# Performance work log

Hardware: AMD Instinct MI355X
Metric: run time of the kernel (lower is better)

## Reference

```python
import jax, jax.numpy as jnp
from jax import lax
import numpy as np

SEQ_LEN, INPUT_DIM, NUM_HIDDEN, NUM_CLASSES, BATCH = 512, 64, 128, 10, 1024


def setup_inputs() -> dict:
    key = jax.random.key(0)
    ks = jax.random.split(key, 12)
    bound = float(np.sqrt(1.0 / NUM_HIDDEN))

    def u(k, shape):
        return jax.random.uniform(k, shape, jnp.float32, -bound, bound)

    return {
        "x": jax.random.normal(ks[0], (BATCH, SEQ_LEN, INPUT_DIM), jnp.float32),
        "W_gx": u(ks[1], (INPUT_DIM, NUM_HIDDEN)),
        "W_gh": u(ks[2], (NUM_HIDDEN, NUM_HIDDEN)),
        "W_ix": u(ks[3], (INPUT_DIM, NUM_HIDDEN)),
        "W_ih": u(ks[4], (NUM_HIDDEN, NUM_HIDDEN)),
        "W_fx": u(ks[5], (INPUT_DIM, NUM_HIDDEN)),
        "W_fh": u(ks[6], (NUM_HIDDEN, NUM_HIDDEN)),
        "W_ox": u(ks[7], (INPUT_DIM, NUM_HIDDEN)),
        "W_oh": u(ks[8], (NUM_HIDDEN, NUM_HIDDEN)),
        "W_ph": u(ks[9], (NUM_HIDDEN, NUM_CLASSES)),
        "b_g": jnp.zeros((NUM_HIDDEN,), jnp.float32),
        "b_i": jnp.zeros((NUM_HIDDEN,), jnp.float32),
        "b_f": jnp.ones((NUM_HIDDEN,), jnp.float32),  # forget-gate bias init to 1 as in original
        "b_o": jnp.zeros((NUM_HIDDEN,), jnp.float32),
        "b_p": jnp.zeros((NUM_CLASSES,), jnp.float32),
    }


def reference(x, W_gx, W_gh, W_ix, W_ih, W_fx, W_fh, W_ox, W_oh, W_ph,
              b_g, b_i, b_f, b_o, b_p):
    B, T, D = x.shape
    H = W_gh.shape[0]

    def step(carry, x_t):  # x_t: [B, D]
        h, c = carry
        g = jnp.tanh(x_t @ W_gx + h @ W_gh + b_g)
        i = jax.nn.sigmoid(x_t @ W_ix + h @ W_ih + b_i)
        f = jax.nn.sigmoid(x_t @ W_fx + h @ W_fh + b_f)
        o = jax.nn.sigmoid(x_t @ W_ox + h @ W_oh + b_o)
        c = g * i + c * f
        h = jnp.tanh(c) * o
        return (h, c), None

    h0 = jnp.zeros((B, H), x.dtype)
    c0 = jnp.zeros((B, H), x.dtype)
    (h, c), _ = lax.scan(step, (h0, c0), jnp.swapaxes(x, 0, 1))  # scan over time
    return h @ W_ph + b_p  # [B, num_classes]
```

## Files before the change

kernel.cpp:

```cpp
#include <hip/hip_runtime.h>

#define BATCH 1024
#define TSEQ  512
#define DIN   64
#define H     128
#define NCLS  10
#define BM    16
#define NTHREADS 512

typedef _Float16 h16;
typedef __attribute__((ext_vector_type(2))) _Float16 half2v;
typedef __attribute__((ext_vector_type(4))) _Float16 half4v;
typedef __attribute__((ext_vector_type(8))) _Float16 half8v;
typedef __attribute__((ext_vector_type(2))) float f32x2;
typedef __attribute__((ext_vector_type(4))) float f32x4;

__device__ __forceinline__ int stg_addr(int m, int k) {
    const int kg = k >> 3;
    return (((kg << 4) + (m ^ (kg & 7))) << 3) + (k & 7);
}

#define SCALE_G (-2.8853900817779268f)
#define SCALE_S (-1.4426950408889634f)

#define MFMA16(A, B, C) __builtin_amdgcn_mfma_f32_16x16x32_f16((A), (B), (C), 0, 0, 0)
#define EXP2(v) __builtin_amdgcn_exp2f(v)
#define RCP(v)  __builtin_amdgcn_rcpf(v)

#define CMATH(ACC, PAIR, CST, YCV)                                              \
  {                                                                             \
    f32x2 eg = { EXP2(ACC[0][2*(PAIR)]), EXP2(ACC[0][2*(PAIR)+1]) };            \
    f32x2 ei = { EXP2(ACC[1][2*(PAIR)]), EXP2(ACC[1][2*(PAIR)+1]) };            \
    f32x2 ef = { EXP2(ACC[2][2*(PAIR)]), EXP2(ACC[2][2*(PAIR)+1]) };            \
    f32x2 ag = one2 + eg, ai = one2 + ei, af = one2 + ef;                       \
    f32x2 dp  = ag * ai;                                                        \
    f32x2 t1  = (one2 - eg) * af;                                               \
    f32x2 num = CST * dp + t1;                                                  \
    f32x2 den = dp * af;                                                        \
    f32x2 rd  = { RCP(den[0]), RCP(den[1]) };                                   \
    f32x2 c   = num * rd;                                                       \
    CST = c;                                                                    \
    f32x2 yc = c * sg2;                                                         \
    YCV[0] = fminf(yc[0], 126.f);                                               \
    YCV[1] = fminf(yc[1], 126.f);                                               \
  }

#define HMATH(ACC, PAIR, YCV)                                                   \
  {                                                                             \
    f32x2 ec = { EXP2(YCV[0]), EXP2(YCV[1]) };                                  \
    f32x2 eo = { EXP2(ACC[3][2*(PAIR)]), EXP2(ACC[3][2*(PAIR)+1]) };            \
    f32x2 dh = (one2 + ec) * (one2 + eo);                                       \
    f32x2 nh = one2 - ec;                                                       \
    f32x2 rh = { RCP(dh[0]), RCP(dh[1]) };                                      \
    f32x2 hv = nh * rh;                                                         \
    hw[hwr[2*(PAIR)]]     = (h16)hv[0];                                         \
    hw[hwr[2*(PAIR) + 1]] = (h16)hv[1];                                         \
  }

__global__ __launch_bounds__(NTHREADS, 2)
void lstm_persist(const float* __restrict__ x,
                  const float* __restrict__ Wgx, const float* __restrict__ Wgh,
                  const float* __restrict__ Wix, const float* __restrict__ Wih,
                  const float* __restrict__ Wfx, const float* __restrict__ Wfh,
                  const float* __restrict__ Wox, const float* __restrict__ Woh,
                  const float* __restrict__ Wph,
                  const float* __restrict__ bg, const float* __restrict__ bi,
                  const float* __restrict__ bfg, const float* __restrict__ bo,
                  const float* __restrict__ bp,
                  float* __restrict__ out)
{
    __shared__ __align__(16) h16 hbuf[2][H * BM];
    __shared__ __align__(16) h16 xbuf[2][DIN * BM];

    const int tid  = threadIdx.x;
    const int wave = tid >> 6;
    const int lane = tid & 63;
    const int grp  = lane >> 4;
    const int ln   = lane & 15;
    const int b0   = blockIdx.x * BM;
    const int n    = (wave << 4) + ln;

    half8v bx[4][2];
    half8v bh[4][4];
    f32x4  bias_c[4];
    {
        const float* WX[4] = {Wgx, Wix, Wfx, Wox};
        const float* WH[4] = {Wgh, Wih, Wfh, Woh};
        const float* BB[4] = {bg, bi, bfg, bo};
        const float  SC[4] = {SCALE_G, SCALE_S, SCALE_S, SCALE_S};
        #pragma unroll
        for (int G = 0; G < 4; ++G) {
            #pragma unroll
            for (int s = 0; s < 2; ++s) {
                half8v v;
                #pragma unroll
                for (int j = 0; j < 8; ++j)
                    v[j] = (h16)(WX[G][(32*s + 8*grp + j) * H + n] * SC[G]);
                bx[G][s] = v;
            }
            #pragma unroll
            for (int s = 0; s < 4; ++s) {
                half8v v;
                #pragma unroll
                for (int j = 0; j < 8; ++j)
                    v[j] = (h16)(WH[G][(32*s + 8*grp + j) * H + n] * SC[G]);
                bh[G][s] = v;
            }
            const float bb = BB[G][n] * SC[G];
            bias_c[G] = (f32x4){bb, bb, bb, bb};
        }
    }

    const int ha0 = stg_addr(ln,      8 * grp);
    const int ha1 = stg_addr(ln, 32 + 8 * grp);
    const int ha2 = stg_addr(ln, 64 + 8 * grp);
    const int ha3 = stg_addr(ln, 96 + 8 * grp);
    const int xa0 = ha0;
    const int xa1 = ha1;
    int hwr[4];
    #pragma unroll
    for (int r = 0; r < 4; ++r) hwr[r] = stg_addr((grp << 2) + r, n);

    const int xm  = tid >> 5;
    const int xk0 = (tid & 31) << 1;
    const int xwr = stg_addr(xm, xk0);
    const float* xrow = x + (size_t)(b0 + xm) * TSEQ * DIN + xk0;

    const f32x2 one2 = {1.f, 1.f};
    const f32x2 sg2  = {SCALE_G, SCALE_G};

    *(half4v*)&hbuf[0][tid << 2] = (half4v)0;
    {
        f32x2 x0 = *(const f32x2*)xrow;
        *(half2v*)&xbuf[0][xwr] =
            __builtin_bit_cast(half2v, __builtin_amdgcn_cvt_pkrtz(x0[0], x0[1]));
    }
    __syncthreads();

    f32x4 accA[4], accB[4];
    {
        half8v xf0 = *(const half8v*)&xbuf[0][xa0];
        half8v xf1 = *(const half8v*)&xbuf[0][xa1];
        #pragma unroll
        for (int G = 0; G < 4; ++G) {
            accA[G] = MFMA16(xf0, bx[G][0], bias_c[G]);
            accA[G] = MFMA16(xf1, bx[G][1], accA[G]);
        }
    }
    __syncthreads();

    f32x2 xhold, xnew;
    {
        f32x2 x1 = *(const f32x2*)(xrow + DIN);
        *(half2v*)&xbuf[0][xwr] =
            __builtin_bit_cast(half2v, __builtin_amdgcn_cvt_pkrtz(x1[0], x1[1]));
        xhold = *(const f32x2*)(xrow + 2 * DIN);
        xnew  = *(const f32x2*)(xrow + 3 * DIN);
    }
    __syncthreads();

    f32x2 cst01 = {0.f, 0.f};
    f32x2 cst23 = {0.f, 0.f};

#define STEP(p_, tcur, ACCC, ACCN)                                              \
  {                                                                             \
                    \
    half8v xf0 = *(const half8v*)&xbuf[p_][xa0];                 \
    half8v xf1 = *(const half8v*)&xbuf[p_][xa1];                                \
    *(half2v*)&xbuf[p_ ^ 1][xwr] =                                              \
        __builtin_bit_cast(half2v, __builtin_amdgcn_cvt_pkrtz(xhold[0], xhold[1])); \
    xhold = xnew;                                                               \
    const int tpre = ((tcur) + 4 < TSEQ) ? (tcur) + 4 : TSEQ - 1;               \
    xnew = *(const f32x2*)(xrow + (size_t)tpre * DIN);                          \
    _Pragma("unroll")                                                           \
    for (int G = 0; G < 4; ++G) {                                               \
        ACCN[G] = MFMA16(xf0, bx[G][0], bias_c[G]);                             \
        ACCN[G] = MFMA16(xf1, bx[G][1], ACCN[G]);                               \
    }                                                                           \
    __syncthreads();                                                            \
                                                       \
    half8v ah0 = *(const half8v*)&hbuf[p_][ha0];                                \
    half8v ah1 = *(const half8v*)&hbuf[p_][ha1];                                \
    half8v ah2 = *(const half8v*)&hbuf[p_][ha2];                                \
    half8v ah3 = *(const half8v*)&hbuf[p_][ha3];                                \
                      \
    ACCC[0] = MFMA16(ah0, bh[0][0], ACCC[0]);                                   \
    ACCC[1] = MFMA16(ah0, bh[1][0], ACCC[1]);                                   \
    ACCC[2] = MFMA16(ah0, bh[2][0], ACCC[2]);                                   \
    ACCC[0] = MFMA16(ah1, bh[0][1], ACCC[0]);                                   \
    ACCC[1] = MFMA16(ah1, bh[1][1], ACCC[1]);                                   \
    ACCC[2] = MFMA16(ah1, bh[2][1], ACCC[2]);                                   \
    ACCC[0] = MFMA16(ah2, bh[0][2], ACCC[0]);                                   \
    ACCC[1] = MFMA16(ah2, bh[1][2], ACCC[1]);                                   \
    ACCC[2] = MFMA16(ah2, bh[2][2], ACCC[2]);                                   \
    ACCC[0] = MFMA16(ah3, bh[0][3], ACCC[0]);                                   \
    ACCC[1] = MFMA16(ah3, bh[1][3], ACCC[1]);                                   \
    ACCC[2] = MFMA16(ah3, bh[2][3], ACCC[2]);                                   \
                             \
    ACCC[3] = MFMA16(ah0, bh[3][0], ACCC[3]);                                   \
    ACCC[3] = MFMA16(ah1, bh[3][1], ACCC[3]);                                   \
    ACCC[3] = MFMA16(ah2, bh[3][2], ACCC[3]);                                   \
    ACCC[3] = MFMA16(ah3, bh[3][3], ACCC[3]);                                   \
    f32x2 yc0, yc1;                                                             \
    CMATH(ACCC, 0, cst01, yc0)                                                  \
    CMATH(ACCC, 1, cst23, yc1)                                                  \
    h16* hw = hbuf[p_ ^ 1];                                                     \
    HMATH(ACCC, 0, yc0)                                                         \
    HMATH(ACCC, 1, yc1)                                                         \
  }

    for (int t = 0; t < TSEQ; t += 2) {
        STEP(0, t,     accA, accB)
        STEP(1, t + 1, accB, accA)
    }
#undef STEP

    __syncthreads();
    if (tid < BM * NCLS) {
        const int m = tid / NCLS;
        const int cls = tid - m * NCLS;
        float s = bp[cls];
        #pragma unroll 8
        for (int k = 0; k < H; ++k) {
            float hvv = (float)hbuf[0][stg_addr(m, k)];
            s += hvv * Wph[k * NCLS + cls];
        }
        out[(size_t)(b0 + m) * NCLS + cls] = s;
    }
}

extern "C" void kernel_launch(void* const* d_in, const int* in_sizes, int n_in,
                              void* d_out, int out_size, void* d_ws, size_t ws_size,
                              hipStream_t stream) {
    (void)in_sizes; (void)n_in; (void)d_ws; (void)ws_size; (void)out_size;
    lstm_persist<<<dim3(BATCH / BM), dim3(NTHREADS), 0, stream>>>(
        (const float*)d_in[0],
        (const float*)d_in[1], (const float*)d_in[2],
        (const float*)d_in[3], (const float*)d_in[4],
        (const float*)d_in[5], (const float*)d_in[6],
        (const float*)d_in[7], (const float*)d_in[8],
        (const float*)d_in[9],
        (const float*)d_in[10], (const float*)d_in[11],
        (const float*)d_in[12], (const float*)d_in[13],
        (const float*)d_in[14],
        (float*)d_out);
}
```

Baseline: 380.2 us.

## Split input projection into producer blocks feeding recurrent consumers via global flags

Adds producer blocks that compute the x-side gate projections for chunks of 16 timesteps into a half-precision workspace buffer and publish each chunk with a release flag. The 64 consumer blocks now only run the recurrent h-matmul and read the precomputed projections, spinning on the flags before each chunk. The aim is to take the input MFMAs and x loads off the serial recurrence critical path. In exchange it adds a large workspace (512 MB), spin-wait synchronisation that relies on producers being co-resident with consumers, and fp16 storage of the pre-activations. A fallback keeps the old kernel when the workspace is too small.

```diff
diff --git a/kernel.cpp b/kernel.cpp
--- a/kernel.cpp
+++ b/kernel.cpp
@@ -7,6 +7,9 @@
 #define NCLS  10
 #define BM    16
 #define NTHREADS 512
+#define NCONS 64
+#define NPROD 192
+#define TSTRIDE ((size_t)64 * 8192)
 
 typedef _Float16 h16;
 typedef __attribute__((ext_vector_type(2))) _Float16 half2v;
@@ -57,132 +60,200 @@
     hw[hwr[2*(PAIR) + 1]] = (h16)hv[1];                                         \
   }
 
+#define CVTACC(ACC, A0, A1)                                                     \
+  {                                                                             \
+    half2v u0 = __builtin_bit_cast(half2v, A0.x);                               \
+    half2v u1 = __builtin_bit_cast(half2v, A0.y);                               \
+    ACC[0] = (f32x4){(float)u0[0], (float)u0[1], (float)u1[0], (float)u1[1]};   \
+    half2v u2 = __builtin_bit_cast(half2v, A0.z);                               \
+    half2v u3 = __builtin_bit_cast(half2v, A0.w);                               \
+    ACC[1] = (f32x4){(float)u2[0], (float)u2[1], (float)u3[0], (float)u3[1]};   \
+    half2v u4 = __builtin_bit_cast(half2v, A1.x);                               \
+    half2v u5 = __builtin_bit_cast(half2v, A1.y);                               \
+    ACC[2] = (f32x4){(float)u4[0], (float)u4[1], (float)u5[0], (float)u5[1]};   \
+    half2v u6 = __builtin_bit_cast(half2v, A1.z);                               \
+    half2v u7 = __builtin_bit_cast(half2v, A1.w);                               \
+    ACC[3] = (f32x4){(float)u6[0], (float)u6[1], (float)u7[0], (float)u7[1]};   \
+  }
+
 __global__ __launch_bounds__(NTHREADS, 2)
-void lstm_persist(const float* __restrict__ x,
-                  const float* __restrict__ Wgx, const float* __restrict__ Wgh,
-                  const float* __restrict__ Wix, const float* __restrict__ Wih,
-                  const float* __restrict__ Wfx, const float* __restrict__ Wfh,
-                  const float* __restrict__ Wox, const float* __restrict__ Woh,
-                  const float* __restrict__ Wph,
-                  const float* __restrict__ bg, const float* __restrict__ bi,
-                  const float* __restrict__ bfg, const float* __restrict__ bo,
-                  const float* __restrict__ bp,
-                  float* __restrict__ out)
+void lstm_fused(const float* __restrict__ x,
+                const float* __restrict__ Wgx, const float* __restrict__ Wgh,
+                const float* __restrict__ Wix, const float* __restrict__ Wih,
+                const float* __restrict__ Wfx, const float* __restrict__ Wfh,
+                const float* __restrict__ Wox, const float* __restrict__ Woh,
+                const float* __restrict__ Wph,
+                const float* __restrict__ bg, const float* __restrict__ bi,
+                const float* __restrict__ bfg, const float* __restrict__ bo,
+                const float* __restrict__ bp,
+                float* __restrict__ out,
+                h16* __restrict__ pre, unsigned* __restrict__ flags)
 {
-    __shared__ __align__(16) h16 hbuf[2][H * BM];
-    __shared__ __align__(16) h16 xbuf[2][DIN * BM];
+    __shared__ __align__(16) h16 smem[8192];
 
     const int tid  = threadIdx.x;
     const int wave = tid >> 6;
     const int lane = tid & 63;
     const int grp  = lane >> 4;
     const int ln   = lane & 15;
-    const int b0   = blockIdx.x * BM;
-    const int n    = (wave << 4) + ln;
-
-    half8v bx[4][2];
+    const float SC[4] = {SCALE_G, SCALE_S, SCALE_S, SCALE_S};
+
+    if (blockIdx.x >= NCONS) {
+        const int pb = blockIdx.x - NCONS;
+        const int b  = pb & 63;
+        const int j  = pb >> 6;
+        const int n  = (wave << 4) + ln;
+
+        half8v bx[4][2];
+        f32x4  bias_c[4];
+        {
+            const float* WX[4] = {Wgx, Wix, Wfx, Wox};
+            const float* BB[4] = {bg, bi, bfg, bo};
+            #pragma unroll
+            for (int G = 0; G < 4; ++G) {
+                #pragma unroll
+                for (int s = 0; s < 2; ++s) {
+                    half8v v;
+                    #pragma unroll
+                    for (int q = 0; q < 8; ++q)
+                        v[q] = (h16)(WX[G][(32*s + 8*grp + q) * H + n] * SC[G]);
+                    bx[G][s] = v;
+                }
+                const float bb = BB[G][n] * SC[G];
+                bias_c[G] = (f32x4){bb, bb, bb, bb};
+            }
+        }
+
+        const int sub  = tid & 63;
+        const int srow = sub >> 2;
+        const int sk0  = (sub & 3) << 4;
+        const int swr0 = stg_addr(srow, sk0);
+        const int swr1 = stg_addr(srow, sk0 + 8);
+        const float* xg0 = x + ((size_t)(b * BM + srow) * TSEQ) * DIN + sk0;
+        const int pxa0 = stg_addr(ln,      8 * grp);
+        const int pxa1 = stg_addr(ln, 32 + 8 * grp);
+        h16* outbase = pre + (size_t)b * 8192 + wave * 1024 + lane * 16;
+
+        for (int c = j; c < 32; c += 3) {
+            #pragma unroll
+            for (int hf = 0; hf < 2; ++hf) {
+                const int t0 = (c << 4) + (hf << 3);
+                __syncthreads();
+                {
+                    const float* xs = xg0 + (size_t)(t0 + wave) * DIN;
+                    f32x4 v0 = *(const f32x4*)(xs);
+                    f32x4 v1 = *(const f32x4*)(xs + 4);
+                    f32x4 v2 = *(const f32x4*)(xs + 8);
+                    f32x4 v3 = *(const f32x4*)(xs + 12);
+                    half8v h0, h1;
+                    #pragma unroll
+                    for (int q = 0; q < 4; ++q) {
+                        h0[q] = (h16)v0[q]; h0[4+q] = (h16)v1[q];
+                        h1[q] = (h16)v2[q]; h1[4+q] = (h16)v3[q];
+                    }
+                    *(half8v*)&smem[wave * 1024 + swr0] = h0;
+                    *(half8v*)&smem[wave * 1024 + swr1] = h1;
+                }
+                __syncthreads();
+                #pragma unroll
+                for (int tt = 0; tt < 8; ++tt) {
+                    half8v ax0 = *(const half8v*)&smem[tt * 1024 + pxa0];
+                    half8v ax1 = *(const half8v*)&smem[tt * 1024 + pxa1];
+                    unsigned u[8];
+                    #pragma unroll
+                    for (int G = 0; G < 4; ++G) {
+                        f32x4 a = MFMA16(ax0, bx[G][0], bias_c[G]);
+                        a = MFMA16(ax1, bx[G][1], a);
+                        u[2*G]   = __builtin_bit_cast(unsigned, __builtin_amdgcn_cvt_pkrtz(a[0], a[1]));
+                        u[2*G+1] = __builtin_bit_cast(unsigned, __builtin_amdgcn_cvt_pkrtz(a[2], a[3]));
+                    }
+                    uint4* dst = (uint4*)(outbase + (size_t)(t0 + tt) * TSTRIDE);
+                    dst[0] = make_uint4(u[0], u[1], u[2], u[3]);
+                    dst[1] = make_uint4(u[4], u[5], u[6], u[7]);
+                }
+            }
+            __threadfence();
+            __syncthreads();
+            if (tid == 0)
+                __hip_atomic_store(&flags[b * 32 + c], 1u,
+                                   __ATOMIC_RELEASE, __HIP_MEMORY_SCOPE_AGENT);
+        }
+        return;
+    }
+
+    const int b  = blockIdx.x;
+    const int b0 = b * BM;
+    const int n  = (wave << 4) + ln;
+
     half8v bh[4][4];
-    f32x4  bias_c[4];
     {
-        const float* WX[4] = {Wgx, Wix, Wfx, Wox};
         const float* WH[4] = {Wgh, Wih, Wfh, Woh};
-        const float* BB[4] = {bg, bi, bfg, bo};
-        const float  SC[4] = {SCALE_G, SCALE_S, SCALE_S, SCALE_S};
         #pragma unroll
-        for (int G = 0; G < 4; ++G) {
-            #pragma unroll
-            for (int s = 0; s < 2; ++s) {
-                half8v v;
-                #pragma unroll
-                for (int j = 0; j < 8; ++j)
-                    v[j] = (h16)(WX[G][(32*s + 8*grp + j) * H + n] * SC[G]);
-                bx[G][s] = v;
-            }
+        for (int G = 0; G < 4; ++G)
             #pragma unroll
             for (int s = 0; s < 4; ++s) {
                 half8v v;
                 #pragma unroll
-                for (int j = 0; j < 8; ++j)
-                    v[j] = (h16)(WH[G][(32*s + 8*grp + j) * H + n] * SC[G]);
+                for (int q = 0; q < 8; ++q)
+                    v[q] = (h16)(WH[G][(32*s + 8*grp + q) * H + n] * SC[G]);
                 bh[G][s] = v;
             }
-            const float bb = BB[G][n] * SC[G];
-            bias_c[G] = (f32x4){bb, bb, bb, bb};
-        }
     }
 
     const int ha0 = stg_addr(ln,      8 * grp);
     const int ha1 = stg_addr(ln, 32 + 8 * grp);
     const int ha2 = stg_addr(ln, 64 + 8 * grp);
     const int ha3 = stg_addr(ln, 96 + 8 * grp);
-    const int xa0 = ha0;
-    const int xa1 = ha1;
     int hwr[4];
     #pragma unroll
     for (int r = 0; r < 4; ++r) hwr[r] = stg_addr((grp << 2) + r, n);
 
-    const int xm  = tid >> 5;
-    const int xk0 = (tid & 31) << 1;
-    const int xwr = stg_addr(xm, xk0);
-    const float* xrow = x + (size_t)(b0 + xm) * TSEQ * DIN + xk0;
-
+    h16* hbuf0 = smem;
+    h16* hbuf1 = smem + 2048;
+    const h16* prelane = pre + (size_t)b * 8192 + wave * 1024 + lane * 16;
+    unsigned* myflags = flags + b * 32;
+
+    if (tid == 0)
+        while (__hip_atomic_load(&myflags[0], __ATOMIC_ACQUIRE,
+                                 __HIP_MEMORY_SCOPE_AGENT) == 0)
+            __builtin_amdgcn_s_sleep(8);
+    __syncthreads();
+    __threadfence();
+
+    *(half4v*)&hbuf0[tid << 2] = (half4v)0;
+    f32x4 accA[4], accB[4];
+    uint4 ph0, ph1, pn0, pn1;
+    {
+        const uint4* q0 = (const uint4*)(prelane);
+        uint4 a0 = q0[0], a1 = q0[1];
+        CVTACC(accA, a0, a1)
+        const uint4* q1 = (const uint4*)(prelane + TSTRIDE);
+        ph0 = q1[0]; ph1 = q1[1];
+        const uint4* q2 = (const uint4*)(prelane + 2 * TSTRIDE);
+        pn0 = q2[0]; pn1 = q2[1];
+    }
+    __syncthreads();
+
+    f32x2 cst01 = {0.f, 0.f};
+    f32x2 cst23 = {0.f, 0.f};
     const f32x2 one2 = {1.f, 1.f};
     const f32x2 sg2  = {SCALE_G, SCALE_G};
 
-    *(half4v*)&hbuf[0][tid << 2] = (half4v)0;
-    {
-        f32x2 x0 = *(const f32x2*)xrow;
-        *(half2v*)&xbuf[0][xwr] =
-            __builtin_bit_cast(half2v, __builtin_amdgcn_cvt_pkrtz(x0[0], x0[1]));
-    }
-    __syncthreads();
-
-    f32x4 accA[4], accB[4];
-    {
-        half8v xf0 = *(const half8v*)&xbuf[0][xa0];
-        half8v xf1 = *(const half8v*)&xbuf[0][xa1];
-        #pragma unroll
-        for (int G = 0; G < 4; ++G) {
-            accA[G] = MFMA16(xf0, bx[G][0], bias_c[G]);
-            accA[G] = MFMA16(xf1, bx[G][1], accA[G]);
-        }
-    }
-    __syncthreads();
-
-    f32x2 xhold, xnew;
-    {
-        f32x2 x1 = *(const f32x2*)(xrow + DIN);
-        *(half2v*)&xbuf[0][xwr] =
-            __builtin_bit_cast(half2v, __builtin_amdgcn_cvt_pkrtz(x1[0], x1[1]));
-        xhold = *(const f32x2*)(xrow + 2 * DIN);
-        xnew  = *(const f32x2*)(xrow + 3 * DIN);
-    }
-    __syncthreads();
-
-    f32x2 cst01 = {0.f, 0.f};
-    f32x2 cst23 = {0.f, 0.f};
-
-#define STEP(p_, tcur, ACCC, ACCN)                                              \
+#define CSTEP(RD, WR, tcur, ACCC, ACCN)                                         \
   {                                                                             \
-                    \
-    half8v xf0 = *(const half8v*)&xbuf[p_][xa0];                 \
-    half8v xf1 = *(const half8v*)&xbuf[p_][xa1];                                \
-    *(half2v*)&xbuf[p_ ^ 1][xwr] =                                              \
-        __builtin_bit_cast(half2v, __builtin_amdgcn_cvt_pkrtz(xhold[0], xhold[1])); \
-    xhold = xnew;                                                               \
-    const int tpre = ((tcur) + 4 < TSEQ) ? (tcur) + 4 : TSEQ - 1;               \
-    xnew = *(const f32x2*)(xrow + (size_t)tpre * DIN);                          \
-    _Pragma("unroll")                                                           \
-    for (int G = 0; G < 4; ++G) {                                               \
-        ACCN[G] = MFMA16(xf0, bx[G][0], bias_c[G]);                             \
-        ACCN[G] = MFMA16(xf1, bx[G][1], ACCN[G]);                               \
+               \
+    CVTACC(ACCN, ph0, ph1)                                                      \
+    ph0 = pn0; ph1 = pn1;                                                       \
+    {                                                                           \
+        const int tld = ((tcur) + 3 < TSEQ) ? (tcur) + 3 : TSEQ - 1;            \
+        const uint4* q = (const uint4*)(prelane + (size_t)tld * TSTRIDE);       \
+        pn0 = q[0]; pn1 = q[1];                                                 \
     }                                                                           \
     __syncthreads();                                                            \
-                                                       \
-    half8v ah0 = *(const half8v*)&hbuf[p_][ha0];                                \
-    half8v ah1 = *(const half8v*)&hbuf[p_][ha1];                                \
-    half8v ah2 = *(const half8v*)&hbuf[p_][ha2];                                \
-    half8v ah3 = *(const half8v*)&hbuf[p_][ha3];                                \
+    half8v ah0 = *(const half8v*)&RD[ha0];                                      \
+    half8v ah1 = *(const half8v*)&RD[ha1];                                      \
+    half8v ah2 = *(const half8v*)&RD[ha2];                                      \
+    half8v ah3 = *(const half8v*)&RD[ha3];                                      \
                       \
     ACCC[0] = MFMA16(ah0, bh[0][0], ACCC[0]);                                   \
     ACCC[1] = MFMA16(ah0, bh[1][0], ACCC[1]);                                   \
@@ -204,6 +275,183 @@
     f32x2 yc0, yc1;                                                             \
     CMATH(ACCC, 0, cst01, yc0)                                                  \
     CMATH(ACCC, 1, cst23, yc1)                                                  \
+    h16* hw = WR;                                                               \
+    HMATH(ACCC, 0, yc0)                                                         \
+    HMATH(ACCC, 1, yc1)                                                         \
+  }
+
+    for (int t = 0; t < TSEQ; t += 2) {
+        if ((t & 15) == 0) {
+            const int cn = (t >> 4) + 1;
+            if (tid == 0 && cn < 32)
+                while (__hip_atomic_load(&myflags[cn], __ATOMIC_ACQUIRE,
+                                         __HIP_MEMORY_SCOPE_AGENT) == 0)
+                    __builtin_amdgcn_s_sleep(8);
+            __syncthreads();
+            __threadfence();
+        }
+        CSTEP(hbuf0, hbuf1, t,     accA, accB)
+        CSTEP(hbuf1, hbuf0, t + 1, accB, accA)
+    }
+#undef CSTEP
+
+    __syncthreads();
+    if (tid < BM * NCLS) {
+        const int m = tid / NCLS;
+        const int cls = tid - m * NCLS;
+        float s = bp[cls];
+        #pragma unroll 8
+        for (int k = 0; k < H; ++k) {
+            float hvv = (float)hbuf0[stg_addr(m, k)];
+            s += hvv * Wph[k * NCLS + cls];
+        }
+        out[(size_t)(b0 + m) * NCLS + cls] = s;
+    }
+}
+
+__global__ __launch_bounds__(NTHREADS, 2)
+void lstm_persist_fb(const float* __restrict__ x,
+                  const float* __restrict__ Wgx, const float* __restrict__ Wgh,
+                  const float* __restrict__ Wix, const float* __restrict__ Wih,
+                  const float* __restrict__ Wfx, const float* __restrict__ Wfh,
+                  const float* __restrict__ Wox, const float* __restrict__ Woh,
+                  const float* __restrict__ Wph,
+                  const float* __restrict__ bg, const float* __restrict__ bi,
+                  const float* __restrict__ bfg, const float* __restrict__ bo,
+                  const float* __restrict__ bp,
+                  float* __restrict__ out)
+{
+    __shared__ __align__(16) h16 hbuf[2][H * BM];
+    __shared__ __align__(16) h16 xbuf[2][DIN * BM];
+
+    const int tid  = threadIdx.x;
+    const int wave = tid >> 6;
+    const int lane = tid & 63;
+    const int grp  = lane >> 4;
+    const int ln   = lane & 15;
+    const int b0   = blockIdx.x * BM;
+    const int n    = (wave << 4) + ln;
+
+    half8v bx[4][2];
+    half8v bh[4][4];
+    f32x4  bias_c[4];
+    {
+        const float* WX[4] = {Wgx, Wix, Wfx, Wox};
+        const float* WH[4] = {Wgh, Wih, Wfh, Woh};
+        const float* BB[4] = {bg, bi, bfg, bo};
+        const float  SC[4] = {SCALE_G, SCALE_S, SCALE_S, SCALE_S};
+        #pragma unroll
+        for (int G = 0; G < 4; ++G) {
+            #pragma unroll
+            for (int s = 0; s < 2; ++s) {
+                half8v v;
+                #pragma unroll
+                for (int q = 0; q < 8; ++q)
+                    v[q] = (h16)(WX[G][(32*s + 8*grp + q) * H + n] * SC[G]);
+                bx[G][s] = v;
+            }
+            #pragma unroll
+            for (int s = 0; s < 4; ++s) {
+                half8v v;
+                #pragma unroll
+                for (int q = 0; q < 8; ++q)
+                    v[q] = (h16)(WH[G][(32*s + 8*grp + q) * H + n] * SC[G]);
+                bh[G][s] = v;
+            }
+            const float bb = BB[G][n] * SC[G];
+            bias_c[G] = (f32x4){bb, bb, bb, bb};
+        }
+    }
+
+    const int ha0 = stg_addr(ln,      8 * grp);
+    const int ha1 = stg_addr(ln, 32 + 8 * grp);
+    const int ha2 = stg_addr(ln, 64 + 8 * grp);
+    const int ha3 = stg_addr(ln, 96 + 8 * grp);
+    const int xa0 = ha0;
+    const int xa1 = ha1;
+    int hwr[4];
+    #pragma unroll
+    for (int r = 0; r < 4; ++r) hwr[r] = stg_addr((grp << 2) + r, n);
+
+    const int xm  = tid >> 5;
+    const int xk0 = (tid & 31) << 1;
+    const int xwr = stg_addr(xm, xk0);
+    const float* xrow = x + (size_t)(b0 + xm) * TSEQ * DIN + xk0;
+
+    const f32x2 one2 = {1.f, 1.f};
+    const f32x2 sg2  = {SCALE_G, SCALE_G};
+
+    *(half4v*)&hbuf[0][tid << 2] = (half4v)0;
+    {
+        f32x2 x0 = *(const f32x2*)xrow;
+        *(half2v*)&xbuf[0][xwr] =
+            __builtin_bit_cast(half2v, __builtin_amdgcn_cvt_pkrtz(x0[0], x0[1]));
+    }
+    __syncthreads();
+
+    f32x4 accA[4], accB[4];
+    {
+        half8v xf0 = *(const half8v*)&xbuf[0][xa0];
+        half8v xf1 = *(const half8v*)&xbuf[0][xa1];
+        #pragma unroll
+        for (int G = 0; G < 4; ++G) {
+            accA[G] = MFMA16(xf0, bx[G][0], bias_c[G]);
+            accA[G] = MFMA16(xf1, bx[G][1], accA[G]);
+        }
+    }
+    __syncthreads();
+
+    f32x2 xhold, xnew;
+    {
+        f32x2 x1 = *(const f32x2*)(xrow + DIN);
+        *(half2v*)&xbuf[0][xwr] =
+            __builtin_bit_cast(half2v, __builtin_amdgcn_cvt_pkrtz(x1[0], x1[1]));
+        xhold = *(const f32x2*)(xrow + 2 * DIN);
+        xnew  = *(const f32x2*)(xrow + 3 * DIN);
+    }
+    __syncthreads();
+
+    f32x2 cst01 = {0.f, 0.f};
+    f32x2 cst23 = {0.f, 0.f};
+
+#define STEP(p_, tcur, ACCC, ACCN)                                              \
+  {                                                                             \
+    half8v xf0 = *(const half8v*)&xbuf[p_][xa0];                                \
+    half8v xf1 = *(const half8v*)&xbuf[p_][xa1];                                \
+    *(half2v*)&xbuf[p_ ^ 1][xwr] =                                              \
+        __builtin_bit_cast(half2v, __builtin_amdgcn_cvt_pkrtz(xhold[0], xhold[1])); \
+    xhold = xnew;                                                               \
+    const int tpre = ((tcur) + 4 < TSEQ) ? (tcur) + 4 : TSEQ - 1;               \
+    xnew = *(const f32x2*)(xrow + (size_t)tpre * DIN);                          \
+    _Pragma("unroll")                                                           \
+    for (int G = 0; G < 4; ++G) {                                               \
+        ACCN[G] = MFMA16(xf0, bx[G][0], bias_c[G]);                             \
+        ACCN[G] = MFMA16(xf1, bx[G][1], ACCN[G]);                               \
+    }                                                                           \
+    __syncthreads();                                                            \
+    half8v ah0 = *(const half8v*)&hbuf[p_][ha0];                                \
+    half8v ah1 = *(const half8v*)&hbuf[p_][ha1];                                \
+    half8v ah2 = *(const half8v*)&hbuf[p_][ha2];                                \
+    half8v ah3 = *(const half8v*)&hbuf[p_][ha3];                                \
+    ACCC[0] = MFMA16(ah0, bh[0][0], ACCC[0]);                                   \
+    ACCC[1] = MFMA16(ah0, bh[1][0], ACCC[1]);                                   \
+    ACCC[2] = MFMA16(ah0, bh[2][0], ACCC[2]);                                   \
+    ACCC[0] = MFMA16(ah1, bh[0][1], ACCC[0]);                                   \
+    ACCC[1] = MFMA16(ah1, bh[1][1], ACCC[1]);                                   \
+    ACCC[2] = MFMA16(ah1, bh[2][1], ACCC[2]);                                   \
+    ACCC[0] = MFMA16(ah2, bh[0][2], ACCC[0]);                                   \
+    ACCC[1] = MFMA16(ah2, bh[1][2], ACCC[1]);                                   \
+    ACCC[2] = MFMA16(ah2, bh[2][2], ACCC[2]);                                   \
+    ACCC[0] = MFMA16(ah3, bh[0][3], ACCC[0]);                                   \
+    ACCC[1] = MFMA16(ah3, bh[1][3], ACCC[1]);                                   \
+    ACCC[2] = MFMA16(ah3, bh[2][3], ACCC[2]);                                   \
+    ACCC[3] = MFMA16(ah0, bh[3][0], ACCC[3]);                                   \
+    ACCC[3] = MFMA16(ah1, bh[3][1], ACCC[3]);                                   \
+    ACCC[3] = MFMA16(ah2, bh[3][2], ACCC[3]);                                   \
+    ACCC[3] = MFMA16(ah3, bh[3][3], ACCC[3]);                                   \
+    f32x2 yc0, yc1;                                                             \
+    CMATH(ACCC, 0, cst01, yc0)                                                  \
+    CMATH(ACCC, 1, cst23, yc1)                                                  \
     h16* hw = hbuf[p_ ^ 1];                                                     \
     HMATH(ACCC, 0, yc0)                                                         \
     HMATH(ACCC, 1, yc1)                                                         \
@@ -232,16 +480,34 @@
 extern "C" void kernel_launch(void* const* d_in, const int* in_sizes, int n_in,
                               void* d_out, int out_size, void* d_ws, size_t ws_size,
                               hipStream_t stream) {
-    (void)in_sizes; (void)n_in; (void)d_ws; (void)ws_size; (void)out_size;
-    lstm_persist<<<dim3(BATCH / BM), dim3(NTHREADS), 0, stream>>>(
-        (const float*)d_in[0],
-        (const float*)d_in[1], (const float*)d_in[2],
-        (const float*)d_in[3], (const float*)d_in[4],
-        (const float*)d_in[5], (const float*)d_in[6],
-        (const float*)d_in[7], (const float*)d_in[8],
-        (const float*)d_in[9],
-        (const float*)d_in[10], (const float*)d_in[11],
-        (const float*)d_in[12], (const float*)d_in[13],
-        (const float*)d_in[14],
-        (float*)d_out);
+    (void)in_sizes; (void)n_in; (void)out_size;
+    const size_t PRE_BYTES  = (size_t)TSEQ * TSTRIDE * 2;
+    const size_t FLAG_BYTES = 8192;
+    if (ws_size >= PRE_BYTES + FLAG_BYTES) {
+        hipMemsetAsync(d_ws, 0, FLAG_BYTES, stream);
+        lstm_fused<<<dim3(NCONS + NPROD), dim3(NTHREADS), 0, stream>>>(
+            (const float*)d_in[0],
+            (const float*)d_in[1], (const float*)d_in[2],
+            (const float*)d_in[3], (const float*)d_in[4],
+            (const float*)d_in[5], (const float*)d_in[6],
+            (const float*)d_in[7], (const float*)d_in[8],
+            (const float*)d_in[9],
+            (const float*)d_in[10], (const float*)d_in[11],
+            (const float*)d_in[12], (const float*)d_in[13],
+            (const float*)d_in[14],
+            (float*)d_out,
+            (h16*)((char*)d_ws + FLAG_BYTES), (unsigned*)d_ws);
+    } else {
+        lstm_persist_fb<<<dim3(BATCH / BM), dim3(NTHREADS), 0, stream>>>(
+            (const float*)d_in[0],
+            (const float*)d_in[1], (const float*)d_in[2],
+            (const float*)d_in[3], (const float*)d_in[4],
+            (const float*)d_in[5], (const float*)d_in[6],
+            (const float*)d_in[7], (const float*)d_in[8],
+            (const float*)d_in[9],
+            (const float*)d_in[10], (const float*)d_in[11],
+            (const float*)d_in[12], (const float*)d_in[13],
+            (const float*)d_in[14],
+            (float*)d_out);
+    }
 }
```

Measured after the change: 378.6 us. About the same (-0.4%).
